# Kernel tuning notes

Hardware: AMD Instinct MI355X
Metric: run time of the kernel (lower is better)

Reference implementation:

```python
import jax, jax.numpy as jnp
import numpy as np

T, C, H, K = 32768, 64, 256, 10
N_LAYERS = 2


def _init(key, shape, scale):
    return jax.random.uniform(key, shape, minval=-scale, maxval=scale, dtype=jnp.float32)


def setup_inputs() -> dict:
    key = jax.random.key(0)
    ks = jax.random.split(key, 32)
    d = {"x": jax.random.normal(ks[0], (T, C), dtype=jnp.float32)}
    i = 1
    in_sz = C
    for l in range(N_LAYERS):
        s = 1.0 / np.sqrt(H)
        for dn in ("f", "b"):
            d[f"w_ih_{dn}{l}"] = _init(ks[i], (3 * H, in_sz), s); i += 1
            d[f"w_hh_{dn}{l}"] = _init(ks[i], (3 * H, H), s); i += 1
            d[f"b_{dn}{l}"] = _init(ks[i], (3 * H,), s); i += 1
            d[f"bn_{dn}{l}"] = _init(ks[i], (H,), s); i += 1
        in_sz = 2 * H
    s2 = 1.0 / np.sqrt(2 * H)
    d["mu_w"] = _init(ks[i], (K, 2 * H), s2); i += 1
    d["mu_b"] = _init(ks[i], (K,), s2); i += 1
    d["sg_w"] = _init(ks[i], (K, 2 * H), s2); i += 1
    d["sg_b"] = _init(ks[i], (K,), s2); i += 1
    return d


def _gru(xs, w_ih, w_hh, b, bn, reverse):
    # Equinox GRUCell math: r,z,n gate order, bias_n added inside r-gated term.
    # Input projections for all timesteps are batched into one GEMM (same math).
    i_all = xs @ w_ih.T + b  # (T, 3H)
    h0 = jnp.zeros(w_hh.shape[1], xs.dtype)

    def step(h, i_t):
        hr, hz, hg = jnp.split(w_hh @ h, 3)
        ir, iz, ig = jnp.split(i_t, 3)
        r = jax.nn.sigmoid(ir + hr)
        z = jax.nn.sigmoid(iz + hz)
        g = jnp.tanh(ig + r * (hg + bn))
        h_new = (1 - z) * g + z * h
        return h_new, h_new

    # reverse=True == scanning xs[::-1] then flipping outputs (original code).
    _, out = jax.lax.scan(step, h0, i_all, reverse=reverse)
    return out  # (T, H)


def reference(x, w_ih_f0, w_hh_f0, b_f0, bn_f0, w_ih_b0, w_hh_b0, b_b0, bn_b0,
              w_ih_f1, w_hh_f1, b_f1, bn_f1, w_ih_b1, w_hh_b1, b_b1, bn_b1,
              mu_w, mu_b, sg_w, sg_b):
    layers = [
        ((w_ih_f0, w_hh_f0, b_f0, bn_f0), (w_ih_b0, w_hh_b0, b_b0, bn_b0)),
        ((w_ih_f1, w_hh_f1, b_f1, bn_f1), (w_ih_b1, w_hh_b1, b_b1, bn_b1)),
    ]
    h = x
    for (pf, pb) in layers:
        out_f = _gru(h, *pf, reverse=False)
        out_b = _gru(h, *pb, reverse=True)
        h = jnp.concatenate([out_f, out_b], axis=-1)  # (T, 2H)
    mu = h @ mu_w.T + mu_b                       # (T, K)
    sigma = jax.nn.softplus(h @ sg_w.T + sg_b)   # (T, K)
    return (mu, sigma)
```

## Files before the change

### kernel.cpp

```cpp
#include <hip/hip_runtime.h>
#include <hip/hip_fp16.h>


typedef _Float16 f16x8 __attribute__((ext_vector_type(8)));
typedef float    f32x4 __attribute__((ext_vector_type(4)));

#define T_LEN 32768
#define HDIM  256

__global__ void cvt_x_kernel(const float* __restrict__ x, __half* __restrict__ xh) {
    int i = (blockIdx.x * 256 + threadIdx.x) * 8;
    f32x4 a = *reinterpret_cast<const f32x4*>(x + i);
    f32x4 b = *reinterpret_cast<const f32x4*>(x + i + 4);
    f16x8 v;
#pragma unroll
    for (int j = 0; j < 4; ++j) { v[j] = (_Float16)a[j]; v[4 + j] = (_Float16)b[j]; }
    *reinterpret_cast<f16x8*>(xh + i) = v;
}

__global__ __launch_bounds__(256, 1)
void gemm_f16_kernel(const __half* __restrict__ A,
                     const float* __restrict__ B0, const float* __restrict__ B1,
                     const float* __restrict__ bias0, const float* __restrict__ bias1,
                     __half* __restrict__ C0, __half* __restrict__ C1, int K) {
    const float* B    = blockIdx.z ? B1 : B0;
    const float* bias = blockIdx.z ? bias1 : bias0;
    __half*      C    = blockIdx.z ? C1 : C0;
    const int m0 = blockIdx.x * 128, n0 = blockIdx.y * 128;
    const int tid = threadIdx.x, lane = tid & 63, wv = tid >> 6;
    const int wm = (wv >> 1) * 64, wn = (wv & 1) * 64;
    const int qq = lane >> 4, r16 = lane & 15;

    __shared__ __align__(16) _Float16 As[128][40];
    __shared__ __align__(16) _Float16 Bs[128][40];

    f32x4 acc[4][4];
#pragma unroll
    for (int i = 0; i < 4; ++i)
#pragma unroll
        for (int j = 0; j < 4; ++j) acc[i][j] = (f32x4){0.f, 0.f, 0.f, 0.f};

    const int r = tid >> 1, seg = tid & 1;
    for (int k0 = 0; k0 < K; k0 += 32) {
        const f16x8* ap = reinterpret_cast<const f16x8*>(A + (size_t)(m0 + r) * K + k0 + 16 * seg);
        f16x8 a0 = ap[0], a1 = ap[1];
        const f32x4* bp = reinterpret_cast<const f32x4*>(B + (size_t)(n0 + r) * K + k0 + 16 * seg);
        f32x4 b0v = bp[0], b1v = bp[1], b2v = bp[2], b3v = bp[3];
        f16x8 bh0, bh1;
#pragma unroll
        for (int j = 0; j < 4; ++j) {
            bh0[j] = (_Float16)b0v[j]; bh0[4 + j] = (_Float16)b1v[j];
            bh1[j] = (_Float16)b2v[j]; bh1[4 + j] = (_Float16)b3v[j];
        }
        *reinterpret_cast<f16x8*>(&As[r][16 * seg])     = a0;
        *reinterpret_cast<f16x8*>(&As[r][16 * seg + 8]) = a1;
        *reinterpret_cast<f16x8*>(&Bs[r][16 * seg])     = bh0;
        *reinterpret_cast<f16x8*>(&Bs[r][16 * seg + 8]) = bh1;
        __syncthreads();

        f16x8 af[4], bf[4];
#pragma unroll
        for (int mi = 0; mi < 4; ++mi)
            af[mi] = *reinterpret_cast<const f16x8*>(&As[wm + 16 * mi + r16][8 * qq]);
#pragma unroll
        for (int ni = 0; ni < 4; ++ni)
            bf[ni] = *reinterpret_cast<const f16x8*>(&Bs[wn + 16 * ni + r16][8 * qq]);
#pragma unroll
        for (int mi = 0; mi < 4; ++mi)
#pragma unroll
            for (int ni = 0; ni < 4; ++ni)
                acc[mi][ni] = __builtin_amdgcn_mfma_f32_16x16x32_f16(af[mi], bf[ni], acc[mi][ni], 0, 0, 0);
        __syncthreads();
    }
#pragma unroll
    for (int mi = 0; mi < 4; ++mi)
#pragma unroll
        for (int ni = 0; ni < 4; ++ni)
#pragma unroll
            for (int rr = 0; rr < 4; ++rr) {
                int grow = m0 + wm + 16 * mi + 4 * qq + rr;
                int gcol = n0 + wn + 16 * ni + r16;
                C[(size_t)grow * 768 + gcol] = __float2half(acc[mi][ni][rr] + bias[gcol]);
            }
}

#define LOAD_X(TP, XR, XZ, XG)                                   \
    {                                                            \
        const __half* ip = iall + (size_t)(TP) * 768;            \
        XR = ip[tid]; XZ = ip[256 + tid]; XG = ip[512 + tid];    \
    }

#define GRU_STEP(P, XR, XZ, XG, TP)                                              \
    {                                                                            \
        const __half* hb = hbuf[P];                                              \
        f16x8 bf[8];                                                             \
        _Pragma("unroll")                                                        \
        for (int kc = 0; kc < 8; ++kc)                                           \
            bf[kc] = *reinterpret_cast<const f16x8*>(hb + kc * 32 + qq * 8);     \
        f32x4 acc[12];                                                           \
        _Pragma("unroll")                                                        \
        for (int i = 0; i < 12; ++i) acc[i] = (f32x4){0.f, 0.f, 0.f, 0.f};       \
        _Pragma("unroll")                                                        \
        for (int kc = 0; kc < 8; ++kc)                                           \
            _Pragma("unroll")                                                    \
            for (int i = 0; i < 12; ++i)                                         \
                acc[i] = __builtin_amdgcn_mfma_f32_16x16x32_f16(a[i][kc], bf[kc], acc[i], 0, 0, 0); \
        if (r16 == 0) {                                                          \
            _Pragma("unroll")                                                    \
            for (int i = 0; i < 12; ++i)                                         \
                *reinterpret_cast<f32x4*>(pre + 16 * (12 * wv + i) + 4 * qq) = acc[i]; \
        }                                                                        \
        asm volatile("s_waitcnt lgkmcnt(0)" ::: "memory");                       \
        __builtin_amdgcn_s_barrier();                                            \
        {                                                                        \
            float pr = pre[tid], pz = pre[256 + tid], pg = pre[512 + tid];       \
            float ar = __half2float(XR) + pr;                                    \
            float az = __half2float(XZ) + pz;                                    \
            float rg = 1.f / (1.f + __expf(-ar));                                \
            float zg = 1.f / (1.f + __expf(-az));                                \
            float ag = __half2float(XG) + rg * (pg + cbn);                       \
            float e2 = __expf(-2.f * fabsf(ag));                                 \
            float th = (1.f - e2) / (1.f + e2);                                  \
            float gg = (ag >= 0.f) ? th : -th;                                   \
            float hn = (1.f - zg) * gg + zg * hold;                              \
            hold = hn;                                                           \
            __half hh = __float2half(hn);                                        \
            hbuf[(P) ^ 1][tid] = hh;                                             \
            out[(size_t)(TP) * 512 + colofs + tid] = hh;                         \
        }                                                                        \
        asm volatile("s_waitcnt lgkmcnt(0)" ::: "memory");                       \
        __builtin_amdgcn_s_barrier();                                            \
    }

__global__ __launch_bounds__(256, 1)
void recur_kernel(const float* __restrict__ whh_f, const float* __restrict__ whh_b,
                  const float* __restrict__ bn_f, const float* __restrict__ bn_b,
                  const __half* __restrict__ iall_f, const __half* __restrict__ iall_b,
                  __half* __restrict__ out ) {
    const int dir = blockIdx.x;
    const float*  whh  = dir ? whh_b  : whh_f;
    const float*  bn   = dir ? bn_b   : bn_f;
    const __half* iall = dir ? iall_b : iall_f;
    const int colofs   = dir ? HDIM : 0;

    const int tid = threadIdx.x;
    const int lane = tid & 63;
    const int wv = tid >> 6;
    const int qq = lane >> 4;
    const int r16 = lane & 15;

    __shared__ __align__(16) __half hbuf[2][HDIM];
    __shared__ __align__(16) float  pre[768];

    f16x8 a[12][8];
#pragma unroll
    for (int i = 0; i < 12; ++i) {
        int row = 16 * (12 * wv + i) + r16;
        const float* wr = whh + (size_t)row * HDIM + 8 * qq;
#pragma unroll
        for (int kc = 0; kc < 8; ++kc) {
            const f32x4* p4 = reinterpret_cast<const f32x4*>(wr + 32 * kc);
            f32x4 w0 = p4[0], w1 = p4[1];
            f16x8 v;
#pragma unroll
            for (int j = 0; j < 4; ++j) { v[j] = (_Float16)w0[j]; v[4 + j] = (_Float16)w1[j]; }
            a[i][kc] = v;
        }
    }
    float cbn = bn[tid];
    float hold = 0.f;
    hbuf[0][tid] = __float2half(0.f);
    __syncthreads();

    __half xr0, xz0, xg0, xr1, xz1, xg1;
    LOAD_X(dir ? T_LEN - 1 : 0, xr0, xz0, xg0);

    for (int ts = 0; ts < T_LEN; ts += 2) {
        const int tp0 = dir ? (T_LEN - 1 - ts) : ts;
        const int tp1 = dir ? (T_LEN - 2 - ts) : ts + 1;
        const int ts2 = (ts + 2 < T_LEN) ? ts + 2 : ts + 1;
        const int tp2 = dir ? (T_LEN - 1 - ts2) : ts2;

        LOAD_X(tp1, xr1, xz1, xg1);
        GRU_STEP(0, xr0, xz0, xg0, tp0);
        LOAD_X(tp2, xr0, xz0, xg0);
        GRU_STEP(1, xr1, xz1, xg1, tp1);
    }
}

__device__ inline float softplus_f(float x) {
    return (x > 20.f) ? x : log1pf(__expf(x));
}

__global__ __launch_bounds__(256, 1)
void head_kernel(const __half* __restrict__ h1,
                 const float* __restrict__ mu_w, const float* __restrict__ mu_b,
                 const float* __restrict__ sg_w, const float* __restrict__ sg_b,
                 float* __restrict__ outp) {
    const int tid = threadIdx.x, lane = tid & 63, wv = tid >> 6;
    const int qq = lane >> 4, r16 = lane & 15;
    const int m0 = blockIdx.x * 128;

    __shared__ __align__(16) _Float16 Ws[32][520];
    __shared__ __align__(16) _Float16 Hs[128][40];

    {
        int rw = tid >> 3, c0 = (tid & 7) * 64;
        const float* src = (rw < 10) ? (mu_w + (size_t)rw * 512 + c0)
                         : (rw < 20) ? (sg_w + (size_t)(rw - 10) * 512 + c0) : nullptr;
        for (int cc = 0; cc < 64; cc += 8) {
            f16x8 hv;
            if (src) {
                f32x4 v0 = *reinterpret_cast<const f32x4*>(src + cc);
                f32x4 v1 = *reinterpret_cast<const f32x4*>(src + cc + 4);
#pragma unroll
                for (int j = 0; j < 4; ++j) { hv[j] = (_Float16)v0[j]; hv[4 + j] = (_Float16)v1[j]; }
            } else {
#pragma unroll
                for (int j = 0; j < 8; ++j) hv[j] = (_Float16)0.f;
            }
            *reinterpret_cast<f16x8*>(&Ws[rw][c0 + cc]) = hv;
        }
    }
    __syncthreads();

    f32x4 acc[2][2];
#pragma unroll
    for (int i = 0; i < 2; ++i)
#pragma unroll
        for (int j = 0; j < 2; ++j) acc[i][j] = (f32x4){0.f, 0.f, 0.f, 0.f};

    const int r = tid >> 1, seg = tid & 1;
    for (int kc = 0; kc < 16; ++kc) {
        const f16x8* hp = reinterpret_cast<const f16x8*>(h1 + (size_t)(m0 + r) * 512 + kc * 32 + 16 * seg);
        f16x8 h0 = hp[0], h1v = hp[1];
        *reinterpret_cast<f16x8*>(&Hs[r][16 * seg])     = h0;
        *reinterpret_cast<f16x8*>(&Hs[r][16 * seg + 8]) = h1v;
        __syncthreads();
        f16x8 af[2], bf[2];
#pragma unroll
        for (int mi = 0; mi < 2; ++mi)
            af[mi] = *reinterpret_cast<const f16x8*>(&Hs[wv * 32 + 16 * mi + r16][8 * qq]);
#pragma unroll
        for (int ni = 0; ni < 2; ++ni)
            bf[ni] = *reinterpret_cast<const f16x8*>(&Ws[16 * ni + r16][kc * 32 + 8 * qq]);
#pragma unroll
        for (int mi = 0; mi < 2; ++mi)
#pragma unroll
            for (int ni = 0; ni < 2; ++ni)
                acc[mi][ni] = __builtin_amdgcn_mfma_f32_16x16x32_f16(af[mi], bf[ni], acc[mi][ni], 0, 0, 0);
        __syncthreads();
    }

#pragma unroll
    for (int mi = 0; mi < 2; ++mi)
#pragma unroll
        for (int ni = 0; ni < 2; ++ni) {
            int ch = 16 * ni + r16;
#pragma unroll
            for (int rr = 0; rr < 4; ++rr) {
                int grow = m0 + wv * 32 + 16 * mi + 4 * qq + rr;
                float v = acc[mi][ni][rr];
                if (ch < 10) {
                    outp[(size_t)grow * 10 + ch] = v + mu_b[ch];
                } else if (ch < 20) {
                    outp[(size_t)T_LEN * 10 + (size_t)grow * 10 + (ch - 10)] = softplus_f(v + sg_b[ch - 10]);
                }
            }
        }
}

extern "C" void kernel_launch(void* const* d_in, const int* in_sizes, int n_in,
                              void* d_out, int out_size, void* d_ws, size_t ws_size,
                              hipStream_t stream) {
    const float* x      = (const float*)d_in[0];
    const float* wih_f0 = (const float*)d_in[1];
    const float* whh_f0 = (const float*)d_in[2];
    const float* b_f0   = (const float*)d_in[3];
    const float* bn_f0  = (const float*)d_in[4];
    const float* wih_b0 = (const float*)d_in[5];
    const float* whh_b0 = (const float*)d_in[6];
    const float* b_b0   = (const float*)d_in[7];
    const float* bn_b0  = (const float*)d_in[8];
    const float* wih_f1 = (const float*)d_in[9];
    const float* whh_f1 = (const float*)d_in[10];
    const float* b_f1   = (const float*)d_in[11];
    const float* bn_f1  = (const float*)d_in[12];
    const float* wih_b1 = (const float*)d_in[13];
    const float* whh_b1 = (const float*)d_in[14];
    const float* b_b1   = (const float*)d_in[15];
    const float* bn_b1  = (const float*)d_in[16];
    const float* mu_w   = (const float*)d_in[17];
    const float* mu_b   = (const float*)d_in[18];
    const float* sg_w   = (const float*)d_in[19];
    const float* sg_b   = (const float*)d_in[20];

    char* ws = (char*)d_ws;
    __half* xh     = (__half*)(ws);
    __half* iall_f = (__half*)(ws + (size_t)4 * 1024 * 1024);
    __half* iall_b = (__half*)(ws + (size_t)52 * 1024 * 1024);
    __half* out0   = (__half*)(ws + (size_t)100 * 1024 * 1024);
    __half* out1   = (__half*)(ws + (size_t)132 * 1024 * 1024);

    cvt_x_kernel<<<dim3((T_LEN * 64) / (256 * 8)), 256, 0, stream>>>(x, xh);
    gemm_f16_kernel<<<dim3(T_LEN / 128, 6, 2), 256, 0, stream>>>(xh, wih_f0, wih_b0, b_f0, b_b0, iall_f, iall_b, 64);
    recur_kernel<<<dim3(2), 256, 0, stream>>>(whh_f0, whh_b0, bn_f0, bn_b0, iall_f, iall_b, out0);
    gemm_f16_kernel<<<dim3(T_LEN / 128, 6, 2), 256, 0, stream>>>(out0, wih_f1, wih_b1, b_f1, b_b1, iall_f, iall_b, 512);
    recur_kernel<<<dim3(2), 256, 0, stream>>>(whh_f1, whh_b1, bn_f1, bn_b1, iall_f, iall_b, out1);
    head_kernel<<<dim3(T_LEN / 128), 256, 0, stream>>>(out1, mu_w, mu_b, sg_w, sg_b, (float*)d_out);
}
```

Baseline: 102.8 ms.

## Spread GRU recurrence over 16 wavefronts and deepen input prefetch

The recurrent kernel now runs 1024 threads per block instead of 256, so each of 16 waves computes only 3 MFMA row tiles of W_hh·h rather than 12. This shortens the serial MFMA chain per timestep on the critical path. The loop is unrolled by four, and the gate-input loads are prefetched four steps ahead in a rotating set of registers. In exchange, each block-wide barrier now synchronizes 16 waves, and only the first 256 threads do the elementwise gate math.

```diff
diff --git a/kernel.cpp b/kernel.cpp
--- a/kernel.cpp
+++ b/kernel.cpp
@@ -84,55 +84,61 @@
             }
 }
 
-#define LOAD_X(TP, XR, XZ, XG)                                   \
-    {                                                            \
-        const __half* ip = iall + (size_t)(TP) * 768;            \
-        XR = ip[tid]; XZ = ip[256 + tid]; XG = ip[512 + tid];    \
-    }
-
-#define GRU_STEP(P, XR, XZ, XG, TP)                                              \
-    {                                                                            \
-        const __half* hb = hbuf[P];                                              \
-        f16x8 bf[8];                                                             \
-        _Pragma("unroll")                                                        \
-        for (int kc = 0; kc < 8; ++kc)                                           \
-            bf[kc] = *reinterpret_cast<const f16x8*>(hb + kc * 32 + qq * 8);     \
-        f32x4 acc[12];                                                           \
-        _Pragma("unroll")                                                        \
-        for (int i = 0; i < 12; ++i) acc[i] = (f32x4){0.f, 0.f, 0.f, 0.f};       \
-        _Pragma("unroll")                                                        \
-        for (int kc = 0; kc < 8; ++kc)                                           \
-            _Pragma("unroll")                                                    \
-            for (int i = 0; i < 12; ++i)                                         \
-                acc[i] = __builtin_amdgcn_mfma_f32_16x16x32_f16(a[i][kc], bf[kc], acc[i], 0, 0, 0); \
-        if (r16 == 0) {                                                          \
-            _Pragma("unroll")                                                    \
-            for (int i = 0; i < 12; ++i)                                         \
-                *reinterpret_cast<f32x4*>(pre + 16 * (12 * wv + i) + 4 * qq) = acc[i]; \
-        }                                                                        \
-        asm volatile("s_waitcnt lgkmcnt(0)" ::: "memory");                       \
-        __builtin_amdgcn_s_barrier();                                            \
-        {                                                                        \
-            float pr = pre[tid], pz = pre[256 + tid], pg = pre[512 + tid];       \
-            float ar = __half2float(XR) + pr;                                    \
-            float az = __half2float(XZ) + pz;                                    \
-            float rg = 1.f / (1.f + __expf(-ar));                                \
-            float zg = 1.f / (1.f + __expf(-az));                                \
-            float ag = __half2float(XG) + rg * (pg + cbn);                       \
-            float e2 = __expf(-2.f * fabsf(ag));                                 \
-            float th = (1.f - e2) / (1.f + e2);                                  \
-            float gg = (ag >= 0.f) ? th : -th;                                   \
-            float hn = (1.f - zg) * gg + zg * hold;                              \
-            hold = hn;                                                           \
-            __half hh = __float2half(hn);                                        \
-            hbuf[(P) ^ 1][tid] = hh;                                             \
-            out[(size_t)(TP) * 512 + colofs + tid] = hh;                         \
-        }                                                                        \
-        asm volatile("s_waitcnt lgkmcnt(0)" ::: "memory");                       \
-        __builtin_amdgcn_s_barrier();                                            \
-    }
-
-__global__ __launch_bounds__(256, 1)
+struct X3 { __half r, z, g; };
+
+#define LOAD_X(DST, TP)                                                \
+    {                                                                  \
+        const __half* ip = iall + (size_t)(TP) * 768;                  \
+        if (tid < HDIM) {                                              \
+            DST.r = ip[tid]; DST.z = ip[256 + tid]; DST.g = ip[512 + tid]; \
+        }                                                              \
+    }
+
+#define GRU_STEP(XS, PB, TP, TPN)                                                 \
+    {                                                                             \
+        __half lxr = XS.r, lxz = XS.z, lxg = XS.g;  \
+        LOAD_X(XS, TPN);                                \
+        const _Float16* hb = &hbuf[PB][0];                                        \
+        f16x8 bf[8];                                                              \
+        _Pragma("unroll")                                                         \
+        for (int kc = 0; kc < 8; ++kc)                                            \
+            bf[kc] = *reinterpret_cast<const f16x8*>(hb + kc * 32 + qq * 8);      \
+        f32x4 acc[3];                                                             \
+        _Pragma("unroll")                                                         \
+        for (int i = 0; i < 3; ++i) acc[i] = (f32x4){0.f, 0.f, 0.f, 0.f};         \
+        _Pragma("unroll")                                                         \
+        for (int kc = 0; kc < 8; ++kc)                                            \
+            _Pragma("unroll")                                                     \
+            for (int i = 0; i < 3; ++i)                                           \
+                acc[i] = __builtin_amdgcn_mfma_f32_16x16x32_f16(aw[i][kc], bf[kc], acc[i], 0, 0, 0); \
+        if (r16 == 0) {                                                           \
+            _Pragma("unroll")                                                     \
+            for (int i = 0; i < 3; ++i)                                           \
+                *reinterpret_cast<f32x4*>(&pre[16 * (3 * wv + i) + 4 * qq]) = acc[i]; \
+        }                                                                         \
+        asm volatile("s_waitcnt lgkmcnt(0)" ::: "memory");                        \
+        __builtin_amdgcn_s_barrier();                                             \
+        if (tid < HDIM) {                                                         \
+            float pr = pre[tid], pz = pre[256 + tid], pg = pre[512 + tid];        \
+            float ar = __half2float(lxr) + pr;                                    \
+            float az = __half2float(lxz) + pz;                                    \
+            float rg = 1.f / (1.f + __expf(-ar));                                 \
+            float zg = 1.f / (1.f + __expf(-az));                                 \
+            float ag = __half2float(lxg) + rg * (pg + cbn);                       \
+            float e2 = __expf(-2.f * fabsf(ag));                                  \
+            float th = (1.f - e2) / (1.f + e2);                                   \
+            float gg = (ag >= 0.f) ? th : -th;                                    \
+            float hn = (1.f - zg) * gg + zg * hold;                               \
+            hold = hn;                                                            \
+            __half hh = __float2half(hn);                                         \
+            hbuf[(PB) ^ 1][tid] = (_Float16)hh;                                   \
+            out[(size_t)(TP) * 512 + colofs + tid] = hh;                          \
+        }                                                                         \
+        asm volatile("s_waitcnt lgkmcnt(0)" ::: "memory");                        \
+        __builtin_amdgcn_s_barrier();                                             \
+    }
+
+__global__ __launch_bounds__(1024, 1)
 void recur_kernel(const float* __restrict__ whh_f, const float* __restrict__ whh_b,
                   const float* __restrict__ bn_f, const float* __restrict__ bn_b,
                   const __half* __restrict__ iall_f, const __half* __restrict__ iall_b,
@@ -144,18 +150,18 @@
     const int colofs   = dir ? HDIM : 0;
 
     const int tid = threadIdx.x;
-    const int lane = tid & 63;
-    const int wv = tid >> 6;
-    const int qq = lane >> 4;
-    const int r16 = lane & 15;
-
-    __shared__ __align__(16) __half hbuf[2][HDIM];
-    __shared__ __align__(16) float  pre[768];
-
-    f16x8 a[12][8];
-#pragma unroll
-    for (int i = 0; i < 12; ++i) {
-        int row = 16 * (12 * wv + i) + r16;
+    const int ln  = tid & 63;
+    const int wv  = tid >> 6;
+    const int qq  = ln >> 4;
+    const int r16 = ln & 15;
+
+    __shared__ __align__(16) _Float16 hbuf[2][HDIM];
+    __shared__ __align__(16) float    pre[768];
+
+    f16x8 aw[3][8];
+#pragma unroll
+    for (int i = 0; i < 3; ++i) {
+        int row = 16 * (3 * wv + i) + r16;
         const float* wr = whh + (size_t)row * HDIM + 8 * qq;
 #pragma unroll
         for (int kc = 0; kc < 8; ++kc) {
@@ -164,27 +170,44 @@
             f16x8 v;
 #pragma unroll
             for (int j = 0; j < 4; ++j) { v[j] = (_Float16)w0[j]; v[4 + j] = (_Float16)w1[j]; }
-            a[i][kc] = v;
+            aw[i][kc] = v;
         }
     }
-    float cbn = bn[tid];
-    float hold = 0.f;
-    hbuf[0][tid] = __float2half(0.f);
+
+    float cbn = 0.f, hold = 0.f;
+    if (tid < HDIM) {
+        cbn = bn[tid];
+        hbuf[0][tid] = (_Float16)0.f;
+    }
     __syncthreads();
 
-    __half xr0, xz0, xg0, xr1, xz1, xg1;
-    LOAD_X(dir ? T_LEN - 1 : 0, xr0, xz0, xg0);
-
-    for (int ts = 0; ts < T_LEN; ts += 2) {
-        const int tp0 = dir ? (T_LEN - 1 - ts) : ts;
-        const int tp1 = dir ? (T_LEN - 2 - ts) : ts + 1;
-        const int ts2 = (ts + 2 < T_LEN) ? ts + 2 : ts + 1;
-        const int tp2 = dir ? (T_LEN - 1 - ts2) : ts2;
-
-        LOAD_X(tp1, xr1, xz1, xg1);
-        GRU_STEP(0, xr0, xz0, xg0, tp0);
-        LOAD_X(tp2, xr0, xz0, xg0);
-        GRU_STEP(1, xr1, xz1, xg1, tp1);
+    X3 s0, s1, s2, s3;
+    {
+        const int t0 = dir ? T_LEN - 1 : 0;
+        const int t1 = dir ? T_LEN - 2 : 1;
+        const int t2 = dir ? T_LEN - 3 : 2;
+        const int t3 = dir ? T_LEN - 4 : 3;
+        LOAD_X(s0, t0); LOAD_X(s1, t1); LOAD_X(s2, t2); LOAD_X(s3, t3);
+    }
+
+    for (int ts = 0; ts < T_LEN; ts += 4) {
+        const int c4 = (ts + 4 < T_LEN) ? ts + 4 : T_LEN - 1;
+        const int c5 = (ts + 5 < T_LEN) ? ts + 5 : T_LEN - 1;
+        const int c6 = (ts + 6 < T_LEN) ? ts + 6 : T_LEN - 1;
+        const int c7 = (ts + 7 < T_LEN) ? ts + 7 : T_LEN - 1;
+        const int tp0 = dir ? (T_LEN - 1 - ts)     : ts;
+        const int tp1 = dir ? (T_LEN - 2 - ts)     : ts + 1;
+        const int tp2 = dir ? (T_LEN - 3 - ts)     : ts + 2;
+        const int tp3 = dir ? (T_LEN - 4 - ts)     : ts + 3;
+        const int tn0 = dir ? (T_LEN - 1 - c4)     : c4;
+        const int tn1 = dir ? (T_LEN - 1 - c5)     : c5;
+        const int tn2 = dir ? (T_LEN - 1 - c6)     : c6;
+        const int tn3 = dir ? (T_LEN - 1 - c7)     : c7;
+
+        GRU_STEP(s0, 0, tp0, tn0);
+        GRU_STEP(s1, 1, tp1, tn1);
+        GRU_STEP(s2, 0, tp2, tn2);
+        GRU_STEP(s3, 1, tp3, tn3);
     }
 }
 
@@ -304,8 +327,8 @@
 
     cvt_x_kernel<<<dim3((T_LEN * 64) / (256 * 8)), 256, 0, stream>>>(x, xh);
     gemm_f16_kernel<<<dim3(T_LEN / 128, 6, 2), 256, 0, stream>>>(xh, wih_f0, wih_b0, b_f0, b_b0, iall_f, iall_b, 64);
-    recur_kernel<<<dim3(2), 256, 0, stream>>>(whh_f0, whh_b0, bn_f0, bn_b0, iall_f, iall_b, out0);
+    recur_kernel<<<dim3(2), 1024, 0, stream>>>(whh_f0, whh_b0, bn_f0, bn_b0, iall_f, iall_b, out0);
     gemm_f16_kernel<<<dim3(T_LEN / 128, 6, 2), 256, 0, stream>>>(out0, wih_f1, wih_b1, b_f1, b_b1, iall_f, iall_b, 512);
-    recur_kernel<<<dim3(2), 256, 0, stream>>>(whh_f1, whh_b1, bn_f1, bn_b1, iall_f, iall_b, out1);
+    recur_kernel<<<dim3(2), 1024, 0, stream>>>(whh_f1, whh_b1, bn_f1, bn_b1, iall_f, iall_b, out1);
     head_kernel<<<dim3(T_LEN / 128), 256, 0, stream>>>(out1, mu_w, mu_b, sg_w, sg_b, (float*)d_out);
 }
```

New measurement: 161.6 ms. 1.57x slower.
